# Optimization experiments

Measured on AMD Instinct MI355X. Metric: run time of the kernel, lower is better.

The kernel has to match this reference:

```python
import jax, jax.numpy as jnp
import numpy as np

B, T, F_DIM, HID, CH = 16, 4096, 47, 64, 256  # batch, frames, feature_dim, hidden_feature_dim, num_channels


def setup_inputs() -> dict:
    key = jax.random.key(0)
    ks = jax.random.split(key, 8)
    s = 0.08  # weight scale
    return {
        "features": jax.random.normal(ks[0], (B, T, F_DIM), jnp.float32),
        # conv1: Conv1d(47, 64, k=1) -> pointwise linear, torch weight (out,in,1) squeezed
        "W1": jax.random.normal(ks[1], (HID, F_DIM), jnp.float32) * s,
        "b1": jnp.zeros((HID,), jnp.float32),
        # conv2: Conv1d(256, 256, k=2), torch weight (out, in, k)
        "W2": jax.random.normal(ks[2], (CH, 4 * HID, 2), jnp.float32) * s,
        "b2": jnp.zeros((CH,), jnp.float32),
        # tconv: ConvTranspose1d(256, 256, k=4, stride=4), torch weight (in, out, k)
        "Wt": jax.random.normal(ks[3], (CH, CH, 4), jnp.float32) * s,
        "bt": jnp.zeros((CH,), jnp.float32),
        # GRU(256, 256), torch layout: (3*H, in) with gate order [r, z, n]
        "W_ih": jax.random.normal(ks[4], (3 * CH, CH), jnp.float32) * s,
        "W_hh": jax.random.normal(ks[5], (3 * CH, CH), jnp.float32) * s,
        "b_ih": jnp.zeros((3 * CH,), jnp.float32),
        "b_hh": jnp.zeros((3 * CH,), jnp.float32),
    }


def reference(features, W1, b1, W2, b2, Wt, bt, W_ih, W_hh, b_ih, b_hh):
    b, t = features.shape[0], features.shape[1]
    ch = Wt.shape[1]
    # conv1 (k=1) == pointwise linear + tanh: (B,T,47) -> (B,T,64)
    c = jnp.tanh(jnp.einsum('btf,hf->bth', features, W1) + b1)
    # group 4 frames: (B, T/4, 256)
    c = c.reshape(b, t // 4, -1)
    # conv2 k=2 with left pad 1 (causal): y[t] = W2[..0] x[t-1] + W2[..1] x[t]
    cp = jnp.pad(c, ((0, 0), (1, 0), (0, 0)))
    c = jnp.tanh(jnp.einsum('bti,oi->bto', cp[:, :-1], W2[:, :, 0])
                 + jnp.einsum('bti,oi->bto', cp[:, 1:], W2[:, :, 1]) + b2)
    # tconv: stride-4 transpose conv, k=4 -> each frame emits 4 steps
    c = jnp.tanh(jnp.einsum('bti,iok->btko', c, Wt) + bt)  # (B, T/4, 4, CH)
    c = c.reshape(b, t, ch)
    # GRU (torch semantics, gate order r,z,n); precompute input projections
    gates_x = jnp.einsum('btc,gc->btg', c, W_ih) + b_ih  # (B,T,3CH)

    def step(h, gx):
        gh = h @ W_hh.T + b_hh
        xr, xz, xn = jnp.split(gx, 3, axis=-1)
        hr, hz, hn = jnp.split(gh, 3, axis=-1)
        r = jax.nn.sigmoid(xr + hr)
        z = jax.nn.sigmoid(xz + hz)
        n = jnp.tanh(xn + r * hn)
        h = (1 - z) * n + z * h
        return h, h

    h0 = jnp.zeros((b, ch), features.dtype)
    _, hs = jax.lax.scan(step, h0, jnp.swapaxes(gates_x, 0, 1))  # (T,B,CH)
    return jnp.swapaxes(hs, 0, 1)  # (B,T,CH)
```

## Files before the change

kernel.cpp:

```cpp
#include <hip/hip_runtime.h>
#include <hip/hip_bf16.h>
#include <stdint.h>

#define B_   16
#define T_   4096
#define F_   47
#define HID_ 64
#define CH_  256
#define TG_  1024
#define G3_  768

using bf16x8 = __attribute__((ext_vector_type(8))) short;
using f32x4  = __attribute__((ext_vector_type(4))) float;

__device__ __forceinline__ short f2bf(float f) {
    union { float f; uint32_t u; } v; v.f = f;
    uint32_t u = v.u;
    uint32_t r = (u + 0x7fffu + ((u >> 16) & 1u)) >> 16;
    return (short)r;
}
__device__ __forceinline__ float bf2f(short s) {
    union { uint32_t u; float f; } v; v.u = ((uint32_t)(uint16_t)s) << 16;
    return v.f;
}
__device__ __forceinline__ float fast_tanh(float x) {
    float e = __expf(2.f * x);
    return 1.f - 2.f / (e + 1.f);
}
__device__ __forceinline__ float fast_sigmoid(float x) {
    return 1.f / (1.f + __expf(-x));
}

__global__ __launch_bounds__(256) void k1_conv1(const float* __restrict__ feat,
        const float* __restrict__ W1, const float* __restrict__ b1,
        short* __restrict__ c1) {
    __shared__ float sW[47 * 64];
    __shared__ float sF[4 * 47];
    int tid = threadIdx.x;
    int b = blockIdx.x >> 10, t0 = (blockIdx.x & 1023) * 4;
    if (tid < 188) sF[tid] = feat[((size_t)b * T_ + t0) * 47 + tid];
    for (int i = tid; i < 47 * 64; i += 256) {
        int f = i >> 6, h = i & 63;
        sW[i] = W1[h * 47 + f];
    }
    __syncthreads();
    int fr = tid >> 6, h = tid & 63;
    float acc = b1[h];
    #pragma unroll
    for (int f = 0; f < 47; ++f)
        acc += sF[fr * 47 + f] * sW[f * 64 + h];
    c1[((size_t)b * T_ + t0 + fr) * 64 + h] = f2bf(fast_tanh(acc));
}

__global__ __launch_bounds__(256) void k_prep(const float* __restrict__ W2,
        const float* __restrict__ Wt, const float* __restrict__ Wih_f,
        short* __restrict__ W2t, short* __restrict__ Wtt, short* __restrict__ Wih) {
    int idx = blockIdx.x * 256 + threadIdx.x;
    if (idx < 256 * 512) {
        int o = idx >> 9, i = idx & 511, d = i >> 8, j = i & 255;
        W2t[idx] = f2bf(W2[(size_t)o * 512 + j * 2 + d]);
    }
    {
        int n = idx >> 8, ic = idx & 255, o = n & 255, kp = n >> 8;
        Wtt[idx] = f2bf(Wt[(size_t)ic * 1024 + o * 4 + kp]);
    }
    if (idx < G3_ * CH_)
        Wih[idx] = f2bf(Wih_f[idx]);
}

__global__ __launch_bounds__(256) void k2_conv2(const short* __restrict__ c1,
        const short* __restrict__ W2t, const float* __restrict__ b2,
        short* __restrict__ y2) {
    int tid = threadIdx.x, w = tid >> 6, l = tid & 63;
    int lane16 = l & 15, quad = l >> 4;
    int mt = blockIdx.x * 4 + w;
    int row = mt * 16 + lane16;
    int tg = row & 1023;
    const short* Arow = c1 + (size_t)row * 256 - 256;
    bf16x8 zero8 = {0,0,0,0,0,0,0,0};
    bf16x8 af[16];
    #pragma unroll
    for (int kt = 0; kt < 16; ++kt) {
        int i0 = kt * 32 + quad * 8;
        bool masked = (tg == 0) && (kt < 8);
        const short* p = masked ? c1 : (Arow + i0);
        bf16x8 v = *(const bf16x8*)p;
        af[kt] = masked ? zero8 : v;
    }
    #pragma unroll
    for (int nt = 0; nt < 16; ++nt) {
        int n = nt * 16 + lane16;
        f32x4 acc = {0.f, 0.f, 0.f, 0.f};
        const short* Brow = W2t + (size_t)n * 512 + quad * 8;
        #pragma unroll
        for (int kt = 0; kt < 16; ++kt) {
            bf16x8 bf = *(const bf16x8*)(Brow + kt * 32);
            acc = __builtin_amdgcn_mfma_f32_16x16x32_bf16(af[kt], bf, acc, 0, 0, 0);
        }
        float bias = b2[n];
        #pragma unroll
        for (int r = 0; r < 4; ++r) {
            int mrow = mt * 16 + quad * 4 + r;
            y2[(size_t)mrow * 256 + n] = f2bf(fast_tanh(acc[r] + bias));
        }
    }
}

__global__ __launch_bounds__(256) void k3a_tconv(const short* __restrict__ y2,
        const short* __restrict__ Wtt, const float* __restrict__ bt,
        short* __restrict__ c3) {
    int tid = threadIdx.x, w = tid >> 6, l = tid & 63;
    int lane16 = l & 15, quad = l >> 4;
    int mt = blockIdx.x;
    int row = mt * 16 + lane16;
    const short* Arow = y2 + (size_t)row * 256 + quad * 8;
    bf16x8 af[8];
    #pragma unroll
    for (int kt = 0; kt < 8; ++kt) af[kt] = *(const bf16x8*)(Arow + kt * 32);
    #pragma unroll
    for (int nt2 = 0; nt2 < 16; ++nt2) {
        int n = (w * 16 + nt2) * 16 + lane16;
        f32x4 acc = {0.f, 0.f, 0.f, 0.f};
        const short* Brow = Wtt + (size_t)n * 256 + quad * 8;
        #pragma unroll
        for (int kt = 0; kt < 8; ++kt) {
            bf16x8 bf = *(const bf16x8*)(Brow + kt * 32);
            acc = __builtin_amdgcn_mfma_f32_16x16x32_bf16(af[kt], bf, acc, 0, 0, 0);
        }
        int kp = n >> 8, o = n & 255;
        float bias = bt[o];
        #pragma unroll
        for (int r = 0; r < 4; ++r) {
            int mrow = mt * 16 + quad * 4 + r;
            int bb = mrow >> 10, tgg = mrow & 1023;
            c3[(((size_t)bb * TG_ + tgg) * 4 + kp) * 256 + o] =
                f2bf(fast_tanh(acc[r] + bias));
        }
    }
}

__global__ __launch_bounds__(256) void k3b_xproj(const short* __restrict__ c3,
        const short* __restrict__ Wih, const float* __restrict__ b_ih,
        short* __restrict__ gates) {
    int tid = threadIdx.x, w = tid >> 6, l = tid & 63;
    int lane16 = l & 15, quad = l >> 4;
    int mt = blockIdx.x;
    int row = mt * 16 + lane16;
    const short* Arow = c3 + (size_t)row * 256 + quad * 8;
    bf16x8 af[8];
    #pragma unroll
    for (int kt = 0; kt < 8; ++kt) af[kt] = *(const bf16x8*)(Arow + kt * 32);
    #pragma unroll
    for (int nt2 = 0; nt2 < 12; ++nt2) {
        int n = (w * 12 + nt2) * 16 + lane16;
        f32x4 acc = {0.f, 0.f, 0.f, 0.f};
        const short* Brow = Wih + (size_t)n * 256 + quad * 8;
        #pragma unroll
        for (int kt = 0; kt < 8; ++kt) {
            bf16x8 bf = *(const bf16x8*)(Brow + kt * 32);
            acc = __builtin_amdgcn_mfma_f32_16x16x32_bf16(af[kt], bf, acc, 0, 0, 0);
        }
        float bias = b_ih[n];
        #pragma unroll
        for (int r = 0; r < 4; ++r) {
            int mrow = mt * 16 + quad * 4 + r;
            gates[(size_t)mrow * G3_ + n] = f2bf(acc[r] + bias);
        }
    }
}

__global__ __launch_bounds__(512, 2) void k4_gru(const float* __restrict__ W_hh,
        const float* __restrict__ b_hh, const short* __restrict__ gates,
        float* __restrict__ out) {
    __shared__ __align__(16) short h_bf[256];
    __shared__ float gh[G3_];
    __shared__ __align__(16) short gxb[2][G3_];
    int tid = threadIdx.x, w = tid >> 6, l = tid & 63;
    int lane16 = l & 15, quad = l >> 4;
    int b = blockIdx.x;

    bf16x8 Bfr[6][8];
    #pragma unroll
    for (int t = 0; t < 6; ++t) {
        int n = (w * 6 + t) * 16 + lane16;
        const float* p = W_hh + (size_t)n * 256 + quad * 8;
        #pragma unroll
        for (int kt = 0; kt < 8; ++kt) {
            const f32x4* q = (const f32x4*)(p + kt * 32);
            f32x4 u0 = q[0], u1 = q[1];
            bf16x8 v;
            v[0] = f2bf(u0[0]); v[1] = f2bf(u0[1]); v[2] = f2bf(u0[2]); v[3] = f2bf(u0[3]);
            v[4] = f2bf(u1[0]); v[5] = f2bf(u1[1]); v[6] = f2bf(u1[2]); v[7] = f2bf(u1[3]);
            Bfr[t][kt] = v;
        }
    }

    float h_reg = 0.f, bhr = 0.f, bhz = 0.f, bhn = 0.f;
    if (tid < 256) {
        h_bf[tid] = 0;
        bhr = b_hh[tid]; bhz = b_hh[256 + tid]; bhn = b_hh[512 + tid];
    }
    const uint32_t* gxg = (const uint32_t*)(gates + (size_t)b * T_ * G3_);
    uint32_t rB = 0, rC = 0;
    if (tid < 384) {
        uint32_t rA = gxg[tid];
        rB = gxg[384 + tid];
        ((uint32_t*)&gxb[0][0])[tid] = rA;
    }
    __syncthreads();

    float* outb = out + (size_t)b * T_ * CH_;
    for (int s = 0; s < T_; ++s) {
        rC = 0;
        if (tid < 384 && s + 2 < T_) rC = gxg[(size_t)(s + 2) * 384 + tid];

        f32x4 acc[6];
        #pragma unroll
        for (int t = 0; t < 6; ++t) acc[t] = (f32x4){0.f, 0.f, 0.f, 0.f};
        bf16x8 a_cur = *(const bf16x8*)&h_bf[quad * 8];
        #pragma unroll
        for (int kt = 0; kt < 8; ++kt) {
            bf16x8 a_nxt = a_cur;
            if (kt < 7) a_nxt = *(const bf16x8*)&h_bf[(kt + 1) * 32 + quad * 8];
            #pragma unroll
            for (int t = 0; t < 6; ++t)
                acc[t] = __builtin_amdgcn_mfma_f32_16x16x32_bf16(a_cur, Bfr[t][kt], acc[t], 0, 0, 0);
            a_cur = a_nxt;
        }
        if (l < 16) {
            #pragma unroll
            for (int t = 0; t < 6; ++t) gh[(w * 6 + t) * 16 + l] = acc[t][0];
        }
        if (tid < 384) ((uint32_t*)&gxb[(s + 1) & 1][0])[tid] = rB;
        __syncthreads();

        if (tid < 256) {
            const short* gx = &gxb[s & 1][0];
            float hr = gh[tid] + bhr;
            float hz = gh[256 + tid] + bhz;
            float hn = gh[512 + tid] + bhn;
            float xr = bf2f(gx[tid]), xz = bf2f(gx[256 + tid]), xn = bf2f(gx[512 + tid]);
            float r = fast_sigmoid(xr + hr);
            float z = fast_sigmoid(xz + hz);
            float nn = fast_tanh(xn + r * hn);
            h_reg = (1.f - z) * nn + z * h_reg;
            h_bf[tid] = f2bf(h_reg);
            outb[(size_t)s * 256 + tid] = h_reg;
        }
        rB = rC;
        __syncthreads();
    }
}

extern "C" void kernel_launch(void* const* d_in, const int* in_sizes, int n_in,
                              void* d_out, int out_size, void* d_ws, size_t ws_size,
                              hipStream_t stream) {
    const float* feat  = (const float*)d_in[0];
    const float* W1    = (const float*)d_in[1];
    const float* b1    = (const float*)d_in[2];
    const float* W2    = (const float*)d_in[3];
    const float* b2    = (const float*)d_in[4];
    const float* Wt    = (const float*)d_in[5];
    const float* bt    = (const float*)d_in[6];
    const float* Wih_f = (const float*)d_in[7];
    const float* Whh   = (const float*)d_in[8];
    const float* bih   = (const float*)d_in[9];
    const float* bhh   = (const float*)d_in[10];
    float* out = (float*)d_out;

    char* ws = (char*)d_ws;
    short* c3    = (short*)(ws);
    short* c1    = (short*)(ws);
    short* gates = (short*)(ws + 33554432);
    short* y2    = (short*)(ws + 33554432);
    short* W2t   = (short*)(ws + 134217728);
    short* Wtt   = (short*)(ws + 134217728 + 262144);
    short* Wih   = (short*)(ws + 134217728 + 262144 + 524288);

    k1_conv1 <<<16384, 256, 0, stream>>>(feat, W1, b1, c1);
    k_prep   <<<1024, 256, 0, stream>>>(W2, Wt, Wih_f, W2t, Wtt, Wih);
    k2_conv2 <<<256,  256, 0, stream>>>(c1, W2t, b2, y2);
    k3a_tconv<<<1024, 256, 0, stream>>>(y2, Wtt, bt, c3);
    k3b_xproj<<<4096, 256, 0, stream>>>(c3, Wih, bih, gates);
    k4_gru   <<<16,   512, 0, stream>>>(Whh, bhh, gates, out);
}
```

Before: 5.488 ms.

## Batch GRU gate prefetch and output stores in 8-step chunks

The GRU recurrence kernel now prefetches input-gate projections for 8 timesteps at once into a larger double-buffered shared array, instead of one step ahead. Hidden states are staged in shared memory and written out as vectorised float4 stores once every 8 steps. The A-fragment loads from h_bf are issued four ahead. The aim is fewer global memory round trips and stores on the serial per-step critical path, at the cost of more shared memory and registers.

```diff
diff --git a/kernel.cpp b/kernel.cpp
--- a/kernel.cpp
+++ b/kernel.cpp
@@ -174,8 +174,10 @@
         float* __restrict__ out) {
     __shared__ __align__(16) short h_bf[256];
     __shared__ float gh[G3_];
-    __shared__ __align__(16) short gxb[2][G3_];
-    int tid = threadIdx.x, w = tid >> 6, l = tid & 63;
+    __shared__ __align__(16) short gxb[2][8][G3_];
+    __shared__ __align__(16) float ob[8][256];
+    int tid = threadIdx.x, l = tid & 63;
+    int w = tid >> 6;
     int lane16 = l & 15, quad = l >> 4;
     int b = blockIdx.x;
 
@@ -201,54 +203,71 @@
         bhr = b_hh[tid]; bhz = b_hh[256 + tid]; bhn = b_hh[512 + tid];
     }
     const uint32_t* gxg = (const uint32_t*)(gates + (size_t)b * T_ * G3_);
-    uint32_t rB = 0, rC = 0;
     if (tid < 384) {
-        uint32_t rA = gxg[tid];
-        rB = gxg[384 + tid];
-        ((uint32_t*)&gxb[0][0])[tid] = rA;
+        #pragma unroll
+        for (int j = 0; j < 8; ++j)
+            ((uint32_t*)&gxb[0][j][0])[tid] = gxg[(size_t)j * 384 + tid];
     }
     __syncthreads();
 
     float* outb = out + (size_t)b * T_ * CH_;
+    uint32_t r[8];
     for (int s = 0; s < T_; ++s) {
-        rC = 0;
-        if (tid < 384 && s + 2 < T_) rC = gxg[(size_t)(s + 2) * 384 + tid];
+        bool ldq = ((s & 7) == 0) && (s + 8 < T_) && (tid < 384);
+        if (ldq) {
+            #pragma unroll
+            for (int j = 0; j < 8; ++j)
+                r[j] = gxg[(size_t)(s + 8 + j) * 384 + tid];
+        }
 
         f32x4 acc[6];
         #pragma unroll
         for (int t = 0; t < 6; ++t) acc[t] = (f32x4){0.f, 0.f, 0.f, 0.f};
-        bf16x8 a_cur = *(const bf16x8*)&h_bf[quad * 8];
+        bf16x8 af[4];
+        #pragma unroll
+        for (int p = 0; p < 4; ++p)
+            af[p] = *(const bf16x8*)&h_bf[p * 32 + quad * 8];
         #pragma unroll
         for (int kt = 0; kt < 8; ++kt) {
-            bf16x8 a_nxt = a_cur;
-            if (kt < 7) a_nxt = *(const bf16x8*)&h_bf[(kt + 1) * 32 + quad * 8];
+            bf16x8 a = af[kt & 3];
+            if (kt + 4 < 8)
+                af[kt & 3] = *(const bf16x8*)&h_bf[(kt + 4) * 32 + quad * 8];
             #pragma unroll
             for (int t = 0; t < 6; ++t)
-                acc[t] = __builtin_amdgcn_mfma_f32_16x16x32_bf16(a_cur, Bfr[t][kt], acc[t], 0, 0, 0);
-            a_cur = a_nxt;
+                acc[t] = __builtin_amdgcn_mfma_f32_16x16x32_bf16(a, Bfr[t][kt], acc[t], 0, 0, 0);
         }
         if (l < 16) {
             #pragma unroll
             for (int t = 0; t < 6; ++t) gh[(w * 6 + t) * 16 + l] = acc[t][0];
         }
-        if (tid < 384) ((uint32_t*)&gxb[(s + 1) & 1][0])[tid] = rB;
         __syncthreads();
 
+        if (ldq) {
+            int half = ((s >> 3) + 1) & 1;
+            #pragma unroll
+            for (int j = 0; j < 8; ++j)
+                ((uint32_t*)&gxb[half][j][0])[tid] = r[j];
+        }
+
         if (tid < 256) {
-            const short* gx = &gxb[s & 1][0];
+            const short* gx = &gxb[(s >> 3) & 1][s & 7][0];
             float hr = gh[tid] + bhr;
             float hz = gh[256 + tid] + bhz;
             float hn = gh[512 + tid] + bhn;
             float xr = bf2f(gx[tid]), xz = bf2f(gx[256 + tid]), xn = bf2f(gx[512 + tid]);
-            float r = fast_sigmoid(xr + hr);
+            float rg = fast_sigmoid(xr + hr);
             float z = fast_sigmoid(xz + hz);
-            float nn = fast_tanh(xn + r * hn);
+            float nn = fast_tanh(xn + rg * hn);
             h_reg = (1.f - z) * nn + z * h_reg;
             h_bf[tid] = f2bf(h_reg);
-            outb[(size_t)s * 256 + tid] = h_reg;
-        }
-        rB = rC;
+            ob[s & 7][tid] = h_reg;
+        }
         __syncthreads();
+
+        if ((s & 7) == 7) {
+            f32x4 v = *(const f32x4*)&ob[0][tid * 4];
+            *(f32x4*)&outb[(size_t)(s - 7) * 256 + tid * 4] = v;
+        }
     }
 }
 
@@ -264,8 +283,8 @@
     const float* bt    = (const float*)d_in[6];
     const float* Wih_f = (const float*)d_in[7];
     const float* Whh   = (const float*)d_in[8];
+    const float* bhh   = (const float*)d_in[10];
     const float* bih   = (const float*)d_in[9];
-    const float* bhh   = (const float*)d_in[10];
     float* out = (float*)d_out;
 
     char* ws = (char*)d_ws;
```

After: 5.678 ms. +3.4%, slower.

## Split GRU hidden dimension across four cooperating blocks with global-memory handoff

Applied to the files above, without the earlier changes.

The GRU recurrence changes from one block per batch element to four blocks. Each block owns 64 hidden channels for all 16 batches, so every MFMA row carries a real batch instead of one useful row in sixteen. Each step's new hidden slices are published through global memory with release/acquire progress flags. Blocks start on their own local k-slice while waiting for peer slices. The input-projection output is relaid out per channel slice, and output writes are batched every four steps. The risks are per-step cross-block synchronisation latency, which may span chiplets, and a bounded spin wait that could time out and proceed with stale state.

```diff
diff --git a/kernel.cpp b/kernel.cpp
--- a/kernel.cpp
+++ b/kernel.cpp
@@ -57,8 +57,8 @@
         short* __restrict__ W2t, short* __restrict__ Wtt, short* __restrict__ Wih) {
     int idx = blockIdx.x * 256 + threadIdx.x;
     if (idx < 256 * 512) {
-        int o = idx >> 9, i = idx & 511, d = i >> 8, j = i & 255;
-        W2t[idx] = f2bf(W2[(size_t)o * 512 + j * 2 + d]);
+        int o = idx >> 9, i = idx & 511, d = i >> 8, jj = i & 255;
+        W2t[idx] = f2bf(W2[(size_t)o * 512 + jj * 2 + d]);
     }
     {
         int n = idx >> 8, ic = idx & 255, o = n & 255, kp = n >> 8;
@@ -141,7 +141,7 @@
 
 __global__ __launch_bounds__(256) void k3b_xproj(const short* __restrict__ c3,
         const short* __restrict__ Wih, const float* __restrict__ b_ih,
-        short* __restrict__ gates) {
+        short* __restrict__ gslice) {
     int tid = threadIdx.x, w = tid >> 6, l = tid & 63;
     int lane16 = l & 15, quad = l >> 4;
     int mt = blockIdx.x;
@@ -161,95 +161,181 @@
             acc = __builtin_amdgcn_mfma_f32_16x16x32_bf16(af[kt], bf, acc, 0, 0, 0);
         }
         float bias = b_ih[n];
+        int gate = n >> 8, rem = n & 255, jj = rem >> 6, cc = rem & 63;
         #pragma unroll
         for (int r = 0; r < 4; ++r) {
             int mrow = mt * 16 + quad * 4 + r;
-            gates[(size_t)mrow * G3_ + n] = f2bf(acc[r] + bias);
-        }
-    }
-}
-
-__global__ __launch_bounds__(512, 2) void k4_gru(const float* __restrict__ W_hh,
-        const float* __restrict__ b_hh, const short* __restrict__ gates,
-        float* __restrict__ out) {
-    __shared__ __align__(16) short h_bf[256];
-    __shared__ float gh[G3_];
-    __shared__ __align__(16) short gxb[2][G3_];
-    int tid = threadIdx.x, w = tid >> 6, l = tid & 63;
+            int bb = mrow >> 12, s = mrow & 4095;
+            gslice[(((size_t)jj * T_ + s) * 16 + bb) * 192 + gate * 64 + cc] =
+                f2bf(acc[r] + bias);
+        }
+    }
+}
+
+__global__ __launch_bounds__(128) void k_zero(int* __restrict__ prog) {
+    prog[threadIdx.x] = 0;
+}
+
+__global__ __launch_bounds__(512) void k4_gru_x4(const float* __restrict__ W_hh,
+        const float* __restrict__ b_hh, const short* __restrict__ gslice,
+        float* __restrict__ out, uint32_t* __restrict__ Hx, int* __restrict__ prog) {
+    __shared__ __align__(16) short h_all[16 * 264];
+    __shared__ float gh_s[16 * 193];
+    __shared__ __align__(16) short gxr[4 * 3072];
+    __shared__ __align__(16) float ob[4 * 1024];
+
+    int tid = threadIdx.x, l = tid & 63, w = tid >> 6;
     int lane16 = l & 15, quad = l >> 4;
-    int b = blockIdx.x;
-
-    bf16x8 Bfr[6][8];
-    #pragma unroll
-    for (int t = 0; t < 6; ++t) {
-        int n = (w * 6 + t) * 16 + lane16;
-        const float* p = W_hh + (size_t)n * 256 + quad * 8;
+    int j = blockIdx.x;
+    bool w4 = (w < 4);
+
+    int t0 = w4 ? w : w;
+    int t1 = w + 8;
+    bf16x8 Bfr0[8], Bfr1[8];
+    {
+        int ng0 = (t0 >> 2) * 256 + j * 64 + (t0 & 3) * 16 + lane16;
+        const float* p0 = W_hh + (size_t)ng0 * 256 + quad * 8;
         #pragma unroll
         for (int kt = 0; kt < 8; ++kt) {
-            const f32x4* q = (const f32x4*)(p + kt * 32);
+            const f32x4* q = (const f32x4*)(p0 + kt * 32);
             f32x4 u0 = q[0], u1 = q[1];
             bf16x8 v;
-            v[0] = f2bf(u0[0]); v[1] = f2bf(u0[1]); v[2] = f2bf(u0[2]); v[3] = f2bf(u0[3]);
-            v[4] = f2bf(u1[0]); v[5] = f2bf(u1[1]); v[6] = f2bf(u1[2]); v[7] = f2bf(u1[3]);
-            Bfr[t][kt] = v;
-        }
-    }
-
-    float h_reg = 0.f, bhr = 0.f, bhz = 0.f, bhn = 0.f;
-    if (tid < 256) {
-        h_bf[tid] = 0;
-        bhr = b_hh[tid]; bhz = b_hh[256 + tid]; bhn = b_hh[512 + tid];
-    }
-    const uint32_t* gxg = (const uint32_t*)(gates + (size_t)b * T_ * G3_);
-    uint32_t rB = 0, rC = 0;
-    if (tid < 384) {
-        uint32_t rA = gxg[tid];
-        rB = gxg[384 + tid];
-        ((uint32_t*)&gxb[0][0])[tid] = rA;
+            v[0]=f2bf(u0[0]); v[1]=f2bf(u0[1]); v[2]=f2bf(u0[2]); v[3]=f2bf(u0[3]);
+            v[4]=f2bf(u1[0]); v[5]=f2bf(u1[1]); v[6]=f2bf(u1[2]); v[7]=f2bf(u1[3]);
+            Bfr0[kt] = v;
+        }
+        if (w4) {
+            int ng1 = (t1 >> 2) * 256 + j * 64 + (t1 & 3) * 16 + lane16;
+            const float* p1 = W_hh + (size_t)ng1 * 256 + quad * 8;
+            #pragma unroll
+            for (int kt = 0; kt < 8; ++kt) {
+                const f32x4* q = (const f32x4*)(p1 + kt * 32);
+                f32x4 u0 = q[0], u1 = q[1];
+                bf16x8 v;
+                v[0]=f2bf(u0[0]); v[1]=f2bf(u0[1]); v[2]=f2bf(u0[2]); v[3]=f2bf(u0[3]);
+                v[4]=f2bf(u1[0]); v[5]=f2bf(u1[1]); v[6]=f2bf(u1[2]); v[7]=f2bf(u1[3]);
+                Bfr1[kt] = v;
+            }
+        }
+    }
+
+    int b0 = tid >> 5, c0 = (tid & 31) * 2;
+    int cg = j * 64 + c0;
+    float bhr0 = b_hh[cg],       bhr1 = b_hh[cg + 1];
+    float bhz0 = b_hh[256 + cg], bhz1 = b_hh[256 + cg + 1];
+    float bhn0 = b_hh[512 + cg], bhn1 = b_hh[512 + cg + 1];
+    float h0 = 0.f, h1 = 0.f;
+
+    for (int v = tid; v < 4096; v += 512)
+        h_all[(v >> 8) * 264 + (v & 255)] = 0;
+    const uint32_t* gsl = (const uint32_t*)(gslice + (size_t)j * T_ * 3072);
+    {
+        #pragma unroll
+        for (int i = 0; i < 12; ++i)
+            ((uint32_t*)gxr)[tid + i * 512] = gsl[tid + i * 512];
     }
     __syncthreads();
 
-    float* outb = out + (size_t)b * T_ * CH_;
+    f32x4 acc0 = {0.f,0.f,0.f,0.f}, acc1 = {0.f,0.f,0.f,0.f};
+
+#define DO_KT(kt) { \
+    bf16x8 a_ = *(const bf16x8*)&h_all[lane16 * 264 + (kt) * 32 + quad * 8]; \
+    acc0 = __builtin_amdgcn_mfma_f32_16x16x32_bf16(a_, Bfr0[kt], acc0, 0, 0, 0); \
+    if (w4) acc1 = __builtin_amdgcn_mfma_f32_16x16x32_bf16(a_, Bfr1[kt], acc1, 0, 0, 0); }
+
     for (int s = 0; s < T_; ++s) {
-        rC = 0;
-        if (tid < 384 && s + 2 < T_) rC = gxg[(size_t)(s + 2) * 384 + tid];
-
-        f32x4 acc[6];
-        #pragma unroll
-        for (int t = 0; t < 6; ++t) acc[t] = (f32x4){0.f, 0.f, 0.f, 0.f};
-        bf16x8 a_cur = *(const bf16x8*)&h_bf[quad * 8];
-        #pragma unroll
-        for (int kt = 0; kt < 8; ++kt) {
-            bf16x8 a_nxt = a_cur;
-            if (kt < 7) a_nxt = *(const bf16x8*)&h_bf[(kt + 1) * 32 + quad * 8];
-            #pragma unroll
-            for (int t = 0; t < 6; ++t)
-                acc[t] = __builtin_amdgcn_mfma_f32_16x16x32_bf16(a_cur, Bfr[t][kt], acc[t], 0, 0, 0);
-            a_cur = a_nxt;
-        }
-        if (l < 16) {
-            #pragma unroll
-            for (int t = 0; t < 6; ++t) gh[(w * 6 + t) * 16 + l] = acc[t][0];
-        }
-        if (tid < 384) ((uint32_t*)&gxb[(s + 1) & 1][0])[tid] = rB;
+        uint32_t pf[12];
+        bool pfs = ((s & 3) == 3) && (s + 4 < T_);
+        if (pfs) {
+            const uint32_t* src = gsl + (size_t)(s + 1) * 1536;
+            #pragma unroll
+            for (int i = 0; i < 12; ++i) pf[i] = src[tid + i * 512];
+        }
+
+        #pragma unroll
+        for (int kt = 0; kt < 8; ++kt)
+            if ((kt >> 1) != j) DO_KT(kt);
+
+        #pragma unroll
+        for (int r = 0; r < 4; ++r) {
+            gh_s[(quad * 4 + r) * 193 + t0 * 16 + lane16] = acc0[r];
+            if (w4) gh_s[(quad * 4 + r) * 193 + t1 * 16 + lane16] = acc1[r];
+        }
         __syncthreads();
 
-        if (tid < 256) {
-            const short* gx = &gxb[s & 1][0];
-            float hr = gh[tid] + bhr;
-            float hz = gh[256 + tid] + bhz;
-            float hn = gh[512 + tid] + bhn;
-            float xr = bf2f(gx[tid]), xz = bf2f(gx[256 + tid]), xn = bf2f(gx[512 + tid]);
-            float r = fast_sigmoid(xr + hr);
-            float z = fast_sigmoid(xz + hz);
-            float nn = fast_tanh(xn + r * hn);
-            h_reg = (1.f - z) * nn + z * h_reg;
-            h_bf[tid] = f2bf(h_reg);
-            outb[(size_t)s * 256 + tid] = h_reg;
-        }
-        rB = rC;
+        uint32_t pi = (s + 1) & 1;
+        {
+            const short* gx = &gxr[(s & 3) * 3072 + b0 * 192];
+            const float* gh = &gh_s[b0 * 193];
+            float r0 = fast_sigmoid(bf2f(gx[c0])      + gh[c0]       + bhr0);
+            float r1 = fast_sigmoid(bf2f(gx[c0 + 1])  + gh[c0 + 1]   + bhr1);
+            float z0 = fast_sigmoid(bf2f(gx[64 + c0]) + gh[64 + c0]  + bhz0);
+            float z1 = fast_sigmoid(bf2f(gx[65 + c0]) + gh[65 + c0]  + bhz1);
+            float n0 = fast_tanh(bf2f(gx[128 + c0]) + r0 * (gh[128 + c0] + bhn0));
+            float n1 = fast_tanh(bf2f(gx[129 + c0]) + r1 * (gh[129 + c0] + bhn1));
+            h0 = (1.f - z0) * n0 + z0 * h0;
+            h1 = (1.f - z1) * n1 + z1 * h1;
+            uint32_t hv = (uint32_t)(uint16_t)f2bf(h0) |
+                          ((uint32_t)(uint16_t)f2bf(h1) << 16);
+            __hip_atomic_store(Hx + (pi * 4 + j) * 512 + tid, hv,
+                               __ATOMIC_RELAXED, __HIP_MEMORY_SCOPE_AGENT);
+            *(uint32_t*)&h_all[b0 * 264 + j * 64 + c0] = hv;
+            float2 hv2; hv2.x = h0; hv2.y = h1;
+            *(float2*)&ob[(s & 3) * 1024 + 2 * tid] = hv2;
+        }
         __syncthreads();
-    }
+
+        if ((s & 3) == 3) {
+            int bA = tid >> 6, c = tid & 63;
+            #pragma unroll
+            for (int k = 0; k < 4; ++k) {
+                size_t so = (size_t)(s - 3 + k) * 256 + j * 64 + c;
+                out[(size_t)bA * (T_ * 256) + so]       = ob[k * 1024 + tid];
+                out[(size_t)(bA + 8) * (T_ * 256) + so] = ob[k * 1024 + 512 + tid];
+            }
+        }
+
+        if (s + 1 < T_) {
+            if (tid == 0)
+                __hip_atomic_store(&prog[j * 32], s + 1,
+                                   __ATOMIC_RELEASE, __HIP_MEMORY_SCOPE_AGENT);
+            if (w == 7 && l < 3) {
+                int x = (j + 1 + (int)l) & 3;
+                int it = 0, v;
+                do {
+                    v = __hip_atomic_load(&prog[x * 32],
+                                          __ATOMIC_ACQUIRE, __HIP_MEMORY_SCOPE_AGENT);
+                } while (v <= s && ++it < 8192);
+            }
+            acc0 = (f32x4){0.f,0.f,0.f,0.f};
+            acc1 = (f32x4){0.f,0.f,0.f,0.f};
+            #pragma unroll
+            for (int kt = 0; kt < 8; ++kt)
+                if ((kt >> 1) == j) DO_KT(kt);
+            __syncthreads();
+
+            uint32_t d[3];
+            #pragma unroll
+            for (int i = 0; i < 3; ++i) {
+                int x = (j + 1 + i) & 3;
+                d[i] = __hip_atomic_load(Hx + (pi * 4 + x) * 512 + tid,
+                                         __ATOMIC_RELAXED, __HIP_MEMORY_SCOPE_AGENT);
+            }
+            #pragma unroll
+            for (int i = 0; i < 3; ++i) {
+                int x = (j + 1 + i) & 3;
+                *(uint32_t*)&h_all[b0 * 264 + x * 64 + c0] = d[i];
+            }
+        }
+
+        if (pfs) {
+            #pragma unroll
+            for (int i = 0; i < 12; ++i)
+                ((uint32_t*)gxr)[tid + i * 512] = pf[i];
+        }
+        __syncthreads();
+    }
+#undef DO_KT
 }
 
 extern "C" void kernel_launch(void* const* d_in, const int* in_sizes, int n_in,
@@ -271,7 +357,9 @@
     char* ws = (char*)d_ws;
     short* c3    = (short*)(ws);
     short* c1    = (short*)(ws);
-    short* gates = (short*)(ws + 33554432);
+    uint32_t* Hx = (uint32_t*)(ws);
+    int* prog    = (int*)(ws + 16384);
+    short* gslice= (short*)(ws + 33554432);
     short* y2    = (short*)(ws + 33554432);
     short* W2t   = (short*)(ws + 134217728);
     short* Wtt   = (short*)(ws + 134217728 + 262144);
@@ -281,6 +369,7 @@
     k_prep   <<<1024, 256, 0, stream>>>(W2, Wt, Wih_f, W2t, Wtt, Wih);
     k2_conv2 <<<256,  256, 0, stream>>>(c1, W2t, b2, y2);
     k3a_tconv<<<1024, 256, 0, stream>>>(y2, Wtt, bt, c3);
-    k3b_xproj<<<4096, 256, 0, stream>>>(c3, Wih, bih, gates);
-    k4_gru   <<<16,   512, 0, stream>>>(Whh, bhh, gates, out);
-}
+    k3b_xproj<<<4096, 256, 0, stream>>>(c3, Wih, bih, gslice);
+    k_zero   <<<1,    128, 0, stream>>>(prog);
+    k4_gru_x4<<<4,    512, 0, stream>>>(Whh, bhh, gslice, out, Hx, prog);
+}
```

Result: slower. 10.46 ms (+90.6%).
